# Kernel tuning notes

Measured on AMD Instinct MI355X. Metric: run time of the kernel, lower is better.

## Reference

```python
import jax, jax.numpy as jnp
import numpy as np

TOP_K = 2


def setup_inputs() -> dict:
    key = jax.random.key(0)
    k1, k2, k3, k4 = jax.random.split(key, 4)
    B, S, D, F, E = 4, 512, 512, 2048, 16
    hidden_states = jax.random.normal(k1, (B, S, D), dtype=jnp.float32)
    gate_weight = jax.random.normal(k2, (E, D), dtype=jnp.float32) * 0.02
    w1 = jax.random.normal(k3, (E, F, D), dtype=jnp.float32) * 0.02
    w2 = jax.random.normal(k4, (E, D, F), dtype=jnp.float32) * 0.02
    return {"hidden_states": hidden_states, "gate_weight": gate_weight, "w1": w1, "w2": w2}


def reference(hidden_states, gate_weight, w1, w2):
    B, S, D = hidden_states.shape
    E = gate_weight.shape[0]
    x = hidden_states.reshape(-1, D)  # [T, D]

    # fused_top_k_routing: logits = x @ Wg^T, top-k, softmax over the k values
    gate_logits = x @ gate_weight.T  # [T, E]
    top_vals, top_idx = jax.lax.top_k(gate_logits, TOP_K)  # [T, k]
    routing_w = jax.nn.softmax(top_vals, axis=-1)  # [T, k]

    # _prepare_expert_inputs: token t goes to expert e iff e in its top-k
    mask = jnp.any(top_idx[:, :, None] == jnp.arange(E)[None, None, :], axis=1)  # [T, E] bool

    # Expert FFN on routed tokens, computed densely over (token, expert) pairs then masked.
    # h[t,e,f] = silu(x_t @ W1_e^T)
    h = jax.nn.silu(jnp.einsum('td,efd->tef', x, w1))  # [T, E, F]
    counts = jnp.sum(mask, axis=0)  # [E]
    h_sum = jnp.einsum('tef,te->ef', h, mask.astype(h.dtype))  # [E, F]
    h_mean = h_sum / jnp.maximum(counts, 1)[:, None].astype(h.dtype)

    # fused_expert_scatter_gather uses expert_outputs[e].mean(dim=0);
    # mean(W2 @ act) = W2 @ mean(act) since W2 is linear.
    y_mean = jnp.einsum('ef,edf->ed', h_mean, w2)  # [E, D]
    y_mean = jnp.where((counts > 0)[:, None], y_mean, 0.0)

    # per-token combine: sum_k w_k * mean_output[expert_k]
    out = jnp.einsum('tk,tkd->td', routing_w, y_mean[top_idx])  # [T, D]
    return out.reshape(B, S, D)
```

## Files before the change

kernel.cpp:

```cpp
#include <hip/hip_runtime.h>

#define NTOK   2048
#define DIM    512
#define FDIM   2048
#define NEXP   16
#define CAP    768
#define BT     256

typedef __bf16 bf16x8 __attribute__((ext_vector_type(8)));
typedef __bf16 bf16x4 __attribute__((ext_vector_type(4)));
typedef float  floatx4 __attribute__((ext_vector_type(4)));

#define WS_COUNTS    0
#define WS_ZEROPAGE  1024
#define WS_TOPIDX    4096
#define WS_ROUTW     20480
#define WS_HMEAN     36864
#define WS_YMEAN     167936
#define WS_XG        200704

__global__ __launch_bounds__(256) void k1_route_gather(
    const float* __restrict__ x, const float* __restrict__ gw,
    int* __restrict__ counts, int* __restrict__ top_idx,
    float* __restrict__ routw, __bf16* __restrict__ Xg)
{
    __shared__ float xt[16 * DIM];
    __shared__ float lg[16][17];
    __shared__ int   gdst[16][2];
    const int tid = threadIdx.x;
    const int t0  = blockIdx.x * 16;

    {
        const float4* src = (const float4*)(x + (size_t)t0 * DIM);
        float4* dst = (float4*)xt;
        #pragma unroll
        for (int i = 0; i < 8; ++i) dst[i * 256 + tid] = src[i * 256 + tid];
    }
    __syncthreads();

    {
        const int tl = tid >> 4, e = tid & 15;
        const float4* xr = (const float4*)(xt + tl * DIM);
        const float4* gr = (const float4*)(gw + e * DIM);
        float acc = 0.f;
        #pragma unroll 8
        for (int j = 0; j < DIM / 4; ++j) {
            float4 a = xr[j], b = gr[j];
            acc += a.x * b.x + a.y * b.y + a.z * b.z + a.w * b.w;
        }
        lg[tl][e] = acc;
    }
    __syncthreads();

    if (tid < 16) {
        const int tl = tid;
        float v0 = -1e30f, v1 = -1e30f; int i0 = 0, i1 = 0;
        #pragma unroll
        for (int e = 0; e < NEXP; ++e) {
            float v = lg[tl][e];
            if (v > v0)      { v1 = v0; i1 = i0; v0 = v; i0 = e; }
            else if (v > v1) { v1 = v;  i1 = e; }
        }
        float e1 = __expf(v1 - v0);
        float w0 = 1.f / (1.f + e1);
        float w1 = 1.f - w0;
        const int t = t0 + tl;
        top_idx[t * 2]     = i0; top_idx[t * 2 + 1] = i1;
        routw[t * 2]       = w0; routw[t * 2 + 1]   = w1;
        int p0 = atomicAdd(counts + i0, 1);
        int p1 = atomicAdd(counts + i1, 1);
        gdst[tl][0] = (p0 < CAP) ? (i0 * CAP + p0) : -1;
        gdst[tl][1] = (p1 < CAP) ? (i1 * CAP + p1) : -1;
    }
    __syncthreads();

    #pragma unroll
    for (int it = 0; it < 16; ++it) {
        int s   = it * 256 + tid;
        int job = s >> 7, el = s & 127;
        int tl  = job >> 1, k = job & 1;
        int dst = gdst[tl][k];
        if (dst >= 0) {
            float4 v = ((const float4*)(xt + tl * DIM))[el];
            bf16x4 o = { (__bf16)v.x, (__bf16)v.y, (__bf16)v.z, (__bf16)v.w };
            *(bf16x4*)(Xg + (size_t)dst * DIM + el * 4) = o;
        }
    }
}

__global__ __launch_bounds__(256) void k2_expert_ffn(
    const float* __restrict__ w1, const __bf16* __restrict__ Xg,
    const int* __restrict__ counts, const __bf16* __restrict__ zp,
    float* __restrict__ hmean)
{
    __shared__ __align__(16) __bf16 w1s[8 * 65 * 8];
    __shared__ __align__(16) __bf16 xs[8 * 257 * 8];
    __shared__ float hred[64][2];

    const int tid  = threadIdx.x;
    const int bid  = blockIdx.x;
    const int e    = bid & 15;
    const int f0   = (bid >> 4) * 64;
    const int cnt  = min(counts[e], CAP);
    const int nblk = (cnt + BT - 1) / BT;
    const float inv = 1.f / (float)max(cnt, 1);

    const int wv   = tid >> 6;
    const int lane = tid & 63;
    const int q    = lane >> 4;
    const int l15  = lane & 15;
    const int fsub = (wv & 1) * 32;
    const int tsub = (wv >> 1) * 128;

    floatx4 acc[2][8];
    float hs[8];
    #pragma unroll
    for (int a = 0; a < 2; ++a)
        #pragma unroll
        for (int b = 0; b < 8; ++b) acc[a][b] = (floatx4)0.f;
    #pragma unroll
    for (int i = 0; i < 8; ++i) hs[i] = 0.f;

    for (int tb = 0; tb < nblk; ++tb) {
        for (int c = 0; c < 8; ++c) {
            const int d0 = c * 64;
            __syncthreads();
            #pragma unroll
            for (int it = 0; it < 2; ++it) {
                int s = it * 256 + tid;
                int f = s >> 3, g = s & 7;
                const float* src = w1 + ((size_t)(e * FDIM + f0 + f)) * DIM + d0 + g * 8;
                float4 a = ((const float4*)src)[0];
                float4 b = ((const float4*)src)[1];
                bf16x8 v;
                v[0] = (__bf16)a.x; v[1] = (__bf16)a.y; v[2] = (__bf16)a.z; v[3] = (__bf16)a.w;
                v[4] = (__bf16)b.x; v[5] = (__bf16)b.y; v[6] = (__bf16)b.z; v[7] = (__bf16)b.w;
                *(bf16x8*)(w1s + ((size_t)g * 65 + f) * 8) = v;
            }
            {
                const int kg = tid & 7;
                const int tb8 = tid >> 3;
                #pragma unroll
                for (int it = 0; it < 8; ++it) {
                    int t = it * 32 + tb8;
                    int r = tb * BT + t;
                    const __bf16* src = (r < cnt)
                        ? (Xg + ((size_t)(e * CAP + r)) * DIM + d0 + kg * 8)
                        : zp;
                    uint4 d = *(const uint4*)src;
                    *(uint4*)(xs + ((size_t)kg * 257 + t) * 8) = d;
                }
            }
            __syncthreads();
            #pragma unroll
            for (int ks = 0; ks < 2; ++ks) {
                const int kg = ks * 4 + q;
                bf16x8 af0 = *(const bf16x8*)(w1s + (kg * 65 + fsub + l15) * 8);
                bf16x8 af1 = *(const bf16x8*)(w1s + (kg * 65 + fsub + 16 + l15) * 8);
                #pragma unroll
                for (int tt = 0; tt < 8; ++tt) {
                    bf16x8 bfr = *(const bf16x8*)(xs + (kg * 257 + tsub + tt * 16 + l15) * 8);
                    acc[0][tt] = __builtin_amdgcn_mfma_f32_16x16x32_bf16(af0, bfr, acc[0][tt], 0, 0, 0);
                    acc[1][tt] = __builtin_amdgcn_mfma_f32_16x16x32_bf16(af1, bfr, acc[1][tt], 0, 0, 0);
                }
            }
        }
        #pragma unroll
        for (int fa = 0; fa < 2; ++fa)
            #pragma unroll
            for (int tt = 0; tt < 8; ++tt)
                #pragma unroll
                for (int r = 0; r < 4; ++r) {
                    float v = acc[fa][tt][r];
                    hs[fa * 4 + r] += v / (1.f + __expf(-v));
                    acc[fa][tt][r] = 0.f;
                }
    }

    #pragma unroll
    for (int i = 0; i < 8; ++i) {
        float v = hs[i];
        v += __shfl_xor(v, 1);
        v += __shfl_xor(v, 2);
        v += __shfl_xor(v, 4);
        v += __shfl_xor(v, 8);
        hs[i] = v;
    }
    if (l15 == 0) {
        #pragma unroll
        for (int fa = 0; fa < 2; ++fa)
            #pragma unroll
            for (int r = 0; r < 4; ++r) {
                int row = fsub + fa * 16 + q * 4 + r;
                hred[row][wv >> 1] = hs[fa * 4 + r];
            }
    }
    __syncthreads();
    if (tid < 64)
        hmean[(size_t)e * FDIM + f0 + tid] = (hred[tid][0] + hred[tid][1]) * inv;
}

__global__ __launch_bounds__(256) void k3_ymean(
    const float* __restrict__ w2, const float* __restrict__ hmean,
    const int* __restrict__ counts, float* __restrict__ ymean)
{
    __shared__ float hl[FDIM];
    const int tid = threadIdx.x;
    const int bid = blockIdx.x;
    const int e   = bid >> 7;
    const int d0  = (bid & 127) * 4;

    {
        const float4* hg = (const float4*)(hmean + (size_t)e * FDIM);
        float4* hl4 = (float4*)hl;
        hl4[tid]       = hg[tid];
        hl4[256 + tid] = hg[256 + tid];
    }
    __syncthreads();

    const int wv = tid >> 6, lane = tid & 63;
    const int d = d0 + wv;
    const float4* wr  = (const float4*)(w2 + ((size_t)e * DIM + d) * FDIM);
    const float4* hl4 = (const float4*)hl;
    float acc = 0.f;
    #pragma unroll
    for (int i = 0; i < 8; ++i) {
        float4 a = wr[i * 64 + lane];
        float4 h = hl4[i * 64 + lane];
        acc += a.x * h.x + a.y * h.y + a.z * h.z + a.w * h.w;
    }
    #pragma unroll
    for (int m = 1; m < 64; m <<= 1) acc += __shfl_xor(acc, m);
    if (lane == 0)
        ymean[e * DIM + d] = (counts[e] > 0) ? acc : 0.f;
}

__global__ __launch_bounds__(256) void k4_combine(
    const int* __restrict__ top_idx, const float* __restrict__ routw,
    const float* __restrict__ ymean, float* __restrict__ out)
{
    const int idx = blockIdx.x * 256 + threadIdx.x;
    const int t = idx >> 7;
    const int c = idx & 127;
    const int i0 = top_idx[t * 2], i1 = top_idx[t * 2 + 1];
    const float w0 = routw[t * 2], w1 = routw[t * 2 + 1];
    float4 a = ((const float4*)(ymean + (size_t)i0 * DIM))[c];
    float4 b = ((const float4*)(ymean + (size_t)i1 * DIM))[c];
    float4 o;
    o.x = w0 * a.x + w1 * b.x;
    o.y = w0 * a.y + w1 * b.y;
    o.z = w0 * a.z + w1 * b.z;
    o.w = w0 * a.w + w1 * b.w;
    ((float4*)out)[idx] = o;
}

extern "C" void kernel_launch(void* const* d_in, const int* in_sizes, int n_in,
                              void* d_out, int out_size, void* d_ws, size_t ws_size,
                              hipStream_t stream)
{
    (void)in_sizes; (void)n_in; (void)out_size; (void)ws_size;
    const float* x  = (const float*)d_in[0];
    const float* gw = (const float*)d_in[1];
    const float* w1 = (const float*)d_in[2];
    const float* w2 = (const float*)d_in[3];
    float* out = (float*)d_out;

    char* ws = (char*)d_ws;
    int*    counts  = (int*)   (ws + WS_COUNTS);
    const __bf16* zp = (const __bf16*)(ws + WS_ZEROPAGE);
    int*    top_idx = (int*)   (ws + WS_TOPIDX);
    float*  routw   = (float*) (ws + WS_ROUTW);
    float*  hmean   = (float*) (ws + WS_HMEAN);
    float*  ymean   = (float*) (ws + WS_YMEAN);
    __bf16* Xg      = (__bf16*)(ws + WS_XG);

    hipMemsetAsync(d_ws, 0, 4096, stream);

    k1_route_gather<<<dim3(NTOK / 16), dim3(256), 0, stream>>>(x, gw, counts, top_idx, routw, Xg);
    k2_expert_ffn  <<<dim3(32 * NEXP), dim3(256), 0, stream>>>(w1, Xg, counts, zp, hmean);
    k3_ymean       <<<dim3(NEXP * 128), dim3(256), 0, stream>>>(w2, hmean, counts, ymean);
    k4_combine     <<<dim3(NTOK * DIM / 4 / 256), dim3(256), 0, stream>>>(top_idx, routw, ymean, out);
}
```

Measured before the change: 231.5 us.

## Split expert FFN token dimension across blocks with atomic hmean accumulation

The expert FFN kernel now launches one block per (token tile of 128, expert, F tile) instead of looping serially over 256-token tiles inside each block. Blocks whose token tile lies beyond the expert's count exit early, and partial SiLU sums are combined into hmean with float atomics. The workspace memset is widened so hmean starts at zero. This raises parallelism beyond 512 blocks, but W1 tiles are reloaded and converted once per token tile, and float atomics make the summation order nondeterministic.

```diff
diff --git a/kernel.cpp b/kernel.cpp
--- a/kernel.cpp
+++ b/kernel.cpp
@@ -5,7 +5,8 @@
 #define FDIM   2048
 #define NEXP   16
 #define CAP    768
-#define BT     256
+#define BT2    128
+#define NTB    (CAP / BT2)
 
 typedef __bf16 bf16x8 __attribute__((ext_vector_type(8)));
 typedef __bf16 bf16x4 __attribute__((ext_vector_type(4)));
@@ -18,6 +19,7 @@
 #define WS_HMEAN     36864
 #define WS_YMEAN     167936
 #define WS_XG        200704
+#define WS_ZERO_BYTES 167936
 
 __global__ __launch_bounds__(256) void k1_route_gather(
     const float* __restrict__ x, const float* __restrict__ gw,
@@ -94,88 +96,88 @@
     float* __restrict__ hmean)
 {
     __shared__ __align__(16) __bf16 w1s[8 * 65 * 8];
-    __shared__ __align__(16) __bf16 xs[8 * 257 * 8];
+    __shared__ __align__(16) __bf16 xs[8 * 129 * 8];
     __shared__ float hred[64][2];
 
-    const int tid  = threadIdx.x;
-    const int bid  = blockIdx.x;
-    const int e    = bid & 15;
-    const int f0   = (bid >> 4) * 64;
-    const int cnt  = min(counts[e], CAP);
-    const int nblk = (cnt + BT - 1) / BT;
-    const float inv = 1.f / (float)max(cnt, 1);
+    const int tid = threadIdx.x;
+    const int bid = blockIdx.x;
+    const int tb  = bid >> 9;
+    const int rem = bid & 511;
+    const int e   = rem & 15;
+    const int f0  = (rem >> 4) * 64;
+    const int cnt = min(counts[e], CAP);
+    if (tb * BT2 >= cnt) return;
+    const float inv = 1.f / (float)cnt;
 
     const int wv   = tid >> 6;
     const int lane = tid & 63;
     const int q    = lane >> 4;
     const int l15  = lane & 15;
     const int fsub = (wv & 1) * 32;
-    const int tsub = (wv >> 1) * 128;
-
-    floatx4 acc[2][8];
+    const int tsub = (wv >> 1) * 64;
+
+    floatx4 acc[2][4];
+    #pragma unroll
+    for (int a = 0; a < 2; ++a)
+        #pragma unroll
+        for (int b = 0; b < 4; ++b) acc[a][b] = (floatx4)0.f;
+
+    for (int c = 0; c < 8; ++c) {
+        const int d0 = c * 64;
+        __syncthreads();
+        #pragma unroll
+        for (int it = 0; it < 2; ++it) {
+            int s = it * 256 + tid;
+            int f = s >> 3, g = s & 7;
+            const float* src = w1 + ((size_t)(e * FDIM + f0 + f)) * DIM + d0 + g * 8;
+            float4 a = ((const float4*)src)[0];
+            float4 b = ((const float4*)src)[1];
+            bf16x8 v;
+            v[0] = (__bf16)a.x; v[1] = (__bf16)a.y; v[2] = (__bf16)a.z; v[3] = (__bf16)a.w;
+            v[4] = (__bf16)b.x; v[5] = (__bf16)b.y; v[6] = (__bf16)b.z; v[7] = (__bf16)b.w;
+            *(bf16x8*)(w1s + ((size_t)g * 65 + f) * 8) = v;
+        }
+        {
+            const int kg = tid & 7;
+            const int r0 = tid >> 3;
+            #pragma unroll
+            for (int it = 0; it < 4; ++it) {
+                int t = it * 32 + r0;
+                int r = tb * BT2 + t;
+                const __bf16* src = (r < cnt)
+                    ? (Xg + ((size_t)(e * CAP + r)) * DIM + d0 + kg * 8)
+                    : zp;
+                uint4 d = *(const uint4*)src;
+                *(uint4*)(xs + ((size_t)kg * 129 + t) * 8) = d;
+            }
+        }
+        __syncthreads();
+        #pragma unroll
+        for (int ks = 0; ks < 2; ++ks) {
+            const int kg = ks * 4 + q;
+            bf16x8 af0 = *(const bf16x8*)(w1s + (kg * 65 + fsub + l15) * 8);
+            bf16x8 af1 = *(const bf16x8*)(w1s + (kg * 65 + fsub + 16 + l15) * 8);
+            #pragma unroll
+            for (int tt = 0; tt < 4; ++tt) {
+                bf16x8 bfr = *(const bf16x8*)(xs + (kg * 129 + tsub + tt * 16 + l15) * 8);
+                acc[0][tt] = __builtin_amdgcn_mfma_f32_16x16x32_bf16(af0, bfr, acc[0][tt], 0, 0, 0);
+                acc[1][tt] = __builtin_amdgcn_mfma_f32_16x16x32_bf16(af1, bfr, acc[1][tt], 0, 0, 0);
+            }
+        }
+    }
+
     float hs[8];
     #pragma unroll
-    for (int a = 0; a < 2; ++a)
-        #pragma unroll
-        for (int b = 0; b < 8; ++b) acc[a][b] = (floatx4)0.f;
-    #pragma unroll
     for (int i = 0; i < 8; ++i) hs[i] = 0.f;
-
-    for (int tb = 0; tb < nblk; ++tb) {
-        for (int c = 0; c < 8; ++c) {
-            const int d0 = c * 64;
-            __syncthreads();
-            #pragma unroll
-            for (int it = 0; it < 2; ++it) {
-                int s = it * 256 + tid;
-                int f = s >> 3, g = s & 7;
-                const float* src = w1 + ((size_t)(e * FDIM + f0 + f)) * DIM + d0 + g * 8;
-                float4 a = ((const float4*)src)[0];
-                float4 b = ((const float4*)src)[1];
-                bf16x8 v;
-                v[0] = (__bf16)a.x; v[1] = (__bf16)a.y; v[2] = (__bf16)a.z; v[3] = (__bf16)a.w;
-                v[4] = (__bf16)b.x; v[5] = (__bf16)b.y; v[6] = (__bf16)b.z; v[7] = (__bf16)b.w;
-                *(bf16x8*)(w1s + ((size_t)g * 65 + f) * 8) = v;
-            }
-            {
-                const int kg = tid & 7;
-                const int tb8 = tid >> 3;
-                #pragma unroll
-                for (int it = 0; it < 8; ++it) {
-                    int t = it * 32 + tb8;
-                    int r = tb * BT + t;
-                    const __bf16* src = (r < cnt)
-                        ? (Xg + ((size_t)(e * CAP + r)) * DIM + d0 + kg * 8)
-                        : zp;
-                    uint4 d = *(const uint4*)src;
-                    *(uint4*)(xs + ((size_t)kg * 257 + t) * 8) = d;
-                }
-            }
-            __syncthreads();
-            #pragma unroll
-            for (int ks = 0; ks < 2; ++ks) {
-                const int kg = ks * 4 + q;
-                bf16x8 af0 = *(const bf16x8*)(w1s + (kg * 65 + fsub + l15) * 8);
-                bf16x8 af1 = *(const bf16x8*)(w1s + (kg * 65 + fsub + 16 + l15) * 8);
-                #pragma unroll
-                for (int tt = 0; tt < 8; ++tt) {
-                    bf16x8 bfr = *(const bf16x8*)(xs + (kg * 257 + tsub + tt * 16 + l15) * 8);
-                    acc[0][tt] = __builtin_amdgcn_mfma_f32_16x16x32_bf16(af0, bfr, acc[0][tt], 0, 0, 0);
-                    acc[1][tt] = __builtin_amdgcn_mfma_f32_16x16x32_bf16(af1, bfr, acc[1][tt], 0, 0, 0);
-                }
-            }
-        }
-        #pragma unroll
-        for (int fa = 0; fa < 2; ++fa)
-            #pragma unroll
-            for (int tt = 0; tt < 8; ++tt)
-                #pragma unroll
-                for (int r = 0; r < 4; ++r) {
-                    float v = acc[fa][tt][r];
-                    hs[fa * 4 + r] += v / (1.f + __expf(-v));
-                    acc[fa][tt][r] = 0.f;
-                }
-    }
+    #pragma unroll
+    for (int fa = 0; fa < 2; ++fa)
+        #pragma unroll
+        for (int tt = 0; tt < 4; ++tt)
+            #pragma unroll
+            for (int r = 0; r < 4; ++r) {
+                float v = acc[fa][tt][r];
+                hs[fa * 4 + r] += v / (1.f + __expf(-v));
+            }
 
     #pragma unroll
     for (int i = 0; i < 8; ++i) {
@@ -197,7 +199,8 @@
     }
     __syncthreads();
     if (tid < 64)
-        hmean[(size_t)e * FDIM + f0 + tid] = (hred[tid][0] + hred[tid][1]) * inv;
+        atomicAdd(hmean + (size_t)e * FDIM + f0 + tid,
+                  (hred[tid][0] + hred[tid][1]) * inv);
 }
 
 __global__ __launch_bounds__(256) void k3_ymean(
@@ -274,10 +277,10 @@
     float*  ymean   = (float*) (ws + WS_YMEAN);
     __bf16* Xg      = (__bf16*)(ws + WS_XG);
 
-    hipMemsetAsync(d_ws, 0, 4096, stream);
+    hipMemsetAsync(d_ws, 0, WS_ZERO_BYTES, stream);
 
     k1_route_gather<<<dim3(NTOK / 16), dim3(256), 0, stream>>>(x, gw, counts, top_idx, routw, Xg);
-    k2_expert_ffn  <<<dim3(32 * NEXP), dim3(256), 0, stream>>>(w1, Xg, counts, zp, hmean);
+    k2_expert_ffn  <<<dim3(NTB * 32 * NEXP), dim3(256), 0, stream>>>(w1, Xg, counts, zp, hmean);
     k3_ymean       <<<dim3(NEXP * 128), dim3(256), 0, stream>>>(w2, hmean, counts, ymean);
     k4_combine     <<<dim3(NTOK * DIM / 4 / 256), dim3(256), 0, stream>>>(top_idx, routw, ymean, out);
 }
```

Measured after the change: 211.1 us. 8.8% less time.
